# Performance work log

Hardware: AMD Instinct MI355X
Metric: run time of the kernel (lower is better)

Reference implementation:

```python
import jax, jax.numpy as jnp
import numpy as np

NUM_HEADS = 16

def setup_inputs() -> dict:
    key = jax.random.key(0)
    k1, k2, k3 = jax.random.split(key, 3)
    B, T, C = 4, 2048, 2048
    x = jax.random.normal(k1, (B, T, C), dtype=jnp.float32)
    Wqkv = jax.random.normal(k2, (C, 3 * C), dtype=jnp.float32) * (C ** -0.5)
    bqkv = jnp.zeros((3 * C,), dtype=jnp.float32)
    Wproj = jax.random.normal(k3, (C, C), dtype=jnp.float32) * (C ** -0.5)
    bproj = jnp.zeros((C,), dtype=jnp.float32)
    return {"x": x, "Wqkv": Wqkv, "bqkv": bqkv, "Wproj": Wproj, "bproj": bproj}

def reference(x, Wqkv, bqkv, Wproj, bproj):
    B, T, C = x.shape
    H = NUM_HEADS
    D = C // H  # head_dim
    qkv = x @ Wqkv + bqkv                      # [B,T,3C]
    q, k, v = jnp.split(qkv, 3, axis=-1)
    # [B,T,C] -> [B,H,T,D]
    q = q.reshape(B, T, H, D).transpose(0, 2, 1, 3)
    k = k.reshape(B, T, H, D).transpose(0, 2, 1, 3)
    v = v.reshape(B, T, H, D).transpose(0, 2, 1, 3)
    scale = D ** -0.5
    scores = jnp.einsum('bhqd,bhkd->bhqk', q, k) * scale  # [B,H,T,T]
    causal = jnp.tril(jnp.ones((T, T), dtype=bool))
    scores = jnp.where(causal, scores, jnp.finfo(scores.dtype).min)
    attn = jax.nn.softmax(scores, axis=-1)
    out = jnp.einsum('bhqk,bhkd->bhqd', attn, v)           # [B,H,T,D]
    out = out.transpose(0, 2, 1, 3).reshape(B, T, C)
    return out @ Wproj + bproj
```

## Files before the change

kernel.cpp:

```cpp
#include <hip/hip_runtime.h>
#include <hip/hip_bf16.h>
#include <stdint.h>

typedef __attribute__((ext_vector_type(8))) short short8;
typedef __attribute__((ext_vector_type(4))) float f32x4;
typedef __attribute__((ext_vector_type(16))) float f32x16;
typedef __attribute__((ext_vector_type(2))) unsigned int uint2v;

__device__ __forceinline__ unsigned short f2bf(float f) {
  union { float f; unsigned int u; } v; v.f = f;
  unsigned int r = v.u + 0x7FFFu + ((v.u >> 16) & 1u);
  return (unsigned short)(r >> 16);
}

__device__ __forceinline__ unsigned int cvtpk(float lo, float hi) {
  unsigned int r;
  asm("v_cvt_pk_bf16_f32 %0, %1, %2" : "=v"(r) : "v"(lo), "v"(hi));
  return r;
}

#define GLOAD16(gsrc, ldst)                                                                  \
  __builtin_amdgcn_global_load_lds((const __attribute__((address_space(1))) void*)(gsrc),    \
                                   (__attribute__((address_space(3))) void*)(ldst), 16, 0, 0)

#define BAR() __builtin_amdgcn_s_barrier()
#define LGKM0() do { asm volatile("s_waitcnt lgkmcnt(0)" ::: "memory"); \
                     __builtin_amdgcn_sched_barrier(0); } while (0)
#define VMCNT0() asm volatile("s_waitcnt vmcnt(0)" ::: "memory")
#define VMCNT8() asm volatile("s_waitcnt vmcnt(8)" ::: "memory")
#define PRIO(x) __builtin_amdgcn_s_setprio(x)

__global__ __launch_bounds__(256) void cast_bf16_kernel(const float* __restrict__ in,
                                                        unsigned short* __restrict__ out) {
  int i = blockIdx.x * 256 + threadIdx.x;
  float4 v = ((const float4*)in)[i];
  ushort4 o;
  o.x = f2bf(v.x); o.y = f2bf(v.y); o.z = f2bf(v.z); o.w = f2bf(v.w);
  ((ushort4*)out)[i] = o;
}

__global__ __launch_bounds__(256) void transpose_cast_kernel(const float* __restrict__ W,
                                                             unsigned short* __restrict__ Wt,
                                                             int K, int N) {
  __shared__ float tile[32][33];
  int n0 = blockIdx.x * 32, k0 = blockIdx.y * 32;
  int tx = threadIdx.x, ty = threadIdx.y;
#pragma unroll
  for (int j = 0; j < 32; j += 8)
    tile[ty + j][tx] = W[(size_t)(k0 + ty + j) * N + n0 + tx];
  __syncthreads();
#pragma unroll
  for (int j = 0; j < 32; j += 8)
    Wt[(size_t)(n0 + ty + j) * K + k0 + tx] = f2bf(tile[tx][ty + j]);
}

__device__ __forceinline__ void stage_half(const unsigned short* __restrict__ gp, int K,
                                           int kt, int half, char* lds_mat, int tid) {
#pragma unroll
  for (int it = 0; it < 2; ++it) {
    int li = half * 1024 + it * 512 + tid;
    int r = li >> 3, c = li & 7;
    int cs = c ^ (r & 7);
    GLOAD16(gp + (size_t)r * K + kt * 64 + cs * 8, lds_mat + li * 16);
  }
}

__device__ __forceinline__ void gemm256_mainloop(const unsigned short* __restrict__ Ap,
                                                 const unsigned short* __restrict__ Bp,
                                                 int K, int tid, char* smem,
                                                 f32x4 acc[8][4]) {
  char* sa = smem;
  char* sb = smem + 65536;
  const int KT = K >> 6;

  int wid = tid >> 6, lane = tid & 63;
  int wr = wid >> 2, wc = wid & 3;
  int lg = lane >> 4, l15 = lane & 15;
  int swz7 = l15 & 7;

  stage_half(Bp, K, 0, 0, sb, tid);
  stage_half(Bp, K, 0, 1, sb, tid);
  stage_half(Ap, K, 0, 0, sa, tid);
  stage_half(Ap, K, 0, 1, sa, tid);
  stage_half(Bp, K, 1, 0, sb + 32768, tid);
  stage_half(Bp, K, 1, 1, sb + 32768, tid);
  stage_half(Ap, K, 1, 0, sa + 32768, tid);
  stage_half(Ap, K, 1, 1, sa + 32768, tid);
  VMCNT8();
  BAR();

#define LDA(ab, m, kc) \
  (*(const short8*)((ab) + (size_t)((wr * 128 + (m) * 16 + l15) * 64 + ((((kc) * 4 + lg) ^ swz7) * 8))))
#define LDB(bb, n, kc) \
  (*(const short8*)((bb) + (size_t)((wc * 64 + (n) * 16 + l15) * 64 + ((((kc) * 4 + lg) ^ swz7) * 8))))

  for (int t = 0; t < KT; ++t) {
    int p = t & 1;
    const unsigned short* ab = (const unsigned short*)(sa + p * 32768);
    const unsigned short* bb = (const unsigned short*)(sb + p * 32768);
    int kt2 = (t + 2 < KT) ? t + 2 : KT - 1;

    short8 bq[4][2], aq[4][2], aq2[4][2];
#pragma unroll
    for (int n = 0; n < 4; ++n) { bq[n][0] = LDB(bb, n, 0); bq[n][1] = LDB(bb, n, 1); }
#pragma unroll
    for (int m = 0; m < 4; ++m) { aq[m][0] = LDA(ab, m, 0); aq[m][1] = LDA(ab, m, 1); }
    BAR();
    LGKM0();
    PRIO(1);
#pragma unroll
    for (int kc = 0; kc < 2; ++kc)
#pragma unroll
      for (int m = 0; m < 4; ++m)
#pragma unroll
        for (int n = 0; n < 2; ++n)
          acc[m][n] = __builtin_amdgcn_mfma_f32_16x16x32_bf16(aq[m][kc], bq[n][kc], acc[m][n], 0, 0, 0);
    PRIO(0);
    BAR();

    stage_half(Bp, K, kt2, 0, sb + p * 32768, tid);
#pragma unroll
    for (int m = 0; m < 4; ++m) { aq2[m][0] = LDA(ab, m + 4, 0); aq2[m][1] = LDA(ab, m + 4, 1); }
    PRIO(1);
#pragma unroll
    for (int kc = 0; kc < 2; ++kc)
#pragma unroll
      for (int m = 0; m < 4; ++m)
#pragma unroll
        for (int n = 2; n < 4; ++n)
          acc[m][n] = __builtin_amdgcn_mfma_f32_16x16x32_bf16(aq[m][kc], bq[n][kc], acc[m][n], 0, 0, 0);
    PRIO(0);

    stage_half(Bp, K, kt2, 1, sb + p * 32768, tid);
    LGKM0();
    PRIO(1);
#pragma unroll
    for (int kc = 0; kc < 2; ++kc)
#pragma unroll
      for (int m = 0; m < 4; ++m)
#pragma unroll
        for (int n = 2; n < 4; ++n)
          acc[m + 4][n] = __builtin_amdgcn_mfma_f32_16x16x32_bf16(aq2[m][kc], bq[n][kc], acc[m + 4][n], 0, 0, 0);
    PRIO(0);
    BAR();

    stage_half(Ap, K, kt2, 0, sa + p * 32768, tid);
    stage_half(Ap, K, kt2, 1, sa + p * 32768, tid);
    PRIO(1);
#pragma unroll
    for (int kc = 0; kc < 2; ++kc)
#pragma unroll
      for (int m = 0; m < 4; ++m)
#pragma unroll
        for (int n = 0; n < 2; ++n)
          acc[m + 4][n] = __builtin_amdgcn_mfma_f32_16x16x32_bf16(aq2[m][kc], bq[n][kc], acc[m + 4][n], 0, 0, 0);
    PRIO(0);
    VMCNT8();
    BAR();
  }
#undef LDA
#undef LDB
}

__global__ __launch_bounds__(512, 2) void gemm_qkv256_kernel(const unsigned short* __restrict__ A,
                                                             const unsigned short* __restrict__ Bt,
                                                             const float* __restrict__ bias,
                                                             unsigned short* __restrict__ qb,
                                                             unsigned short* __restrict__ kb,
                                                             unsigned short* __restrict__ vtb) {
  extern __shared__ char smem[];
  int wg = blockIdx.x;
  int xcd = wg & 7, idx = wg >> 3;
  int bn = xcd * 3 + idx % 3;
  int bm = idx / 3;
  int tid = threadIdx.x;

  f32x4 acc[8][4];
  f32x4 zero = {0.f, 0.f, 0.f, 0.f};
#pragma unroll
  for (int m = 0; m < 8; ++m)
#pragma unroll
    for (int n = 0; n < 4; ++n) acc[m][n] = zero;

  gemm256_mainloop(A + (size_t)bm * 256 * 2048, Bt + (size_t)bn * 256 * 2048, 2048, tid, smem, acc);

  const float QSCALE = (float)(0.08838834764831845 * 1.4426950408889634);
  int wid = tid >> 6, lane = tid & 63;
  int wr = wid >> 2, wc = wid & 3, lg = lane >> 4, l15 = lane & 15;
  int l31 = lane & 31, hi = lane >> 5;

  if (bn >= 16) {
    VMCNT0();
    BAR();
#pragma unroll
    for (int n = 0; n < 4; ++n) {
      int cl = wc * 64 + n * 16 + l15;
      float bv = bias[bn * 256 + cl];
#pragma unroll
      for (int m = 0; m < 8; ++m) {
        int rl = wr * 128 + m * 16 + lg * 4;
        unsigned int w0 = cvtpk(acc[m][n][0] + bv, acc[m][n][1] + bv);
        unsigned int w1 = cvtpk(acc[m][n][2] + bv, acc[m][n][3] + bv);
        uint2v pk = {w0, w1};
        *(uint2v*)(smem + cl * 512 + ((rl * 2) ^ ((cl & 7) << 4))) = pk;
      }
    }
    LGKM0();
    BAR();
    int t0_abs = bm * 256;
    int bq_ = t0_abs >> 11, t0 = t0_abs & 2047;
    int h0 = (bn * 256 - 4096) >> 7;
#pragma unroll
    for (int i = 0; i < 16; ++i) {
      int dloc = i * 16 + wid * 2 + hi;
      short8 vrow = *(const short8*)(smem + dloc * 512 + ((l31 * 16) ^ ((dloc & 7) << 4)));
      int bh_ = bq_ * 16 + h0 + (dloc >> 7);
      int d = dloc & 127;
      *(short8*)(vtb + ((size_t)bh_ * 128 + d) * 2048 + t0 + l31 * 8) = vrow;
    }
  } else {
#pragma unroll
    for (int n = 0; n < 4; ++n) {
      int col = bn * 256 + wc * 64 + n * 16 + l15;
      float bv = bias[col];
      int which = col >> 11;
      int h = (col & 2047) >> 7;
      int d = col & 127;
#pragma unroll
      for (int m = 0; m < 8; ++m) {
#pragma unroll
        for (int g = 0; g < 4; ++g) {
          int row = bm * 256 + wr * 128 + m * 16 + lg * 4 + g;
          int b = row >> 11, t = row & 2047;
          float r = acc[m][n][g] + bv;
          if (which == 0) r *= QSCALE;
          unsigned short val = f2bf(r);
          size_t bhi = (size_t)(b * 16 + h);
          if (which == 0) qb[(bhi * 2048 + t) * 128 + d] = val;
          else            kb[(bhi * 2048 + t) * 128 + d] = val;
        }
      }
    }
  }
}

__global__ __launch_bounds__(512, 2) void gemm_proj256_kernel(const unsigned short* __restrict__ A,
                                                              const unsigned short* __restrict__ Bt,
                                                              const float* __restrict__ bias,
                                                              float* __restrict__ out) {
  extern __shared__ char smem[];
  int wg = blockIdx.x;
  int bm = wg >> 3, bn = wg & 7;
  int tid = threadIdx.x;

  f32x4 acc[8][4];
  f32x4 zero = {0.f, 0.f, 0.f, 0.f};
#pragma unroll
  for (int m = 0; m < 8; ++m)
#pragma unroll
    for (int n = 0; n < 4; ++n) acc[m][n] = zero;

  gemm256_mainloop(A + (size_t)bm * 256 * 2048, Bt + (size_t)bn * 256 * 2048, 2048, tid, smem, acc);

  int wid = tid >> 6, lane = tid & 63;
  int wr = wid >> 2, wc = wid & 3, lg = lane >> 4, l15 = lane & 15;
#pragma unroll
  for (int n = 0; n < 4; ++n) {
    int col = bn * 256 + wc * 64 + n * 16 + l15;
    float bv = bias[col];
#pragma unroll
    for (int m = 0; m < 8; ++m) {
#pragma unroll
      for (int g = 0; g < 4; ++g) {
        int row = bm * 256 + wr * 128 + m * 16 + lg * 4 + g;
        out[(size_t)row * 2048 + col] = acc[m][n][g] + bv;
      }
    }
  }
}

__global__ __launch_bounds__(256) void attn_kernel(const unsigned short* __restrict__ qb,
                                                   const unsigned short* __restrict__ kb,
                                                   const unsigned short* __restrict__ vtb,
                                                   unsigned short* __restrict__ ob) {
  extern __shared__ char asmem[];
  int pairi = blockIdx.x;
  int bh = blockIdx.y;
  int b = bh >> 4, h = bh & 15;
  int tid = threadIdx.x, wid = tid >> 6, lane = tid & 63;
  int l31 = lane & 31, hi = lane >> 5;

  const unsigned short* Q  = qb  + (size_t)bh * 2048 * 128;
  const unsigned short* K  = kb  + (size_t)bh * 2048 * 128;
  const unsigned short* Vt = vtb + (size_t)bh * 128 * 2048;

#pragma unroll 1
  for (int pass = 0; pass < 2; ++pass) {
    int qt = pass == 0 ? (15 - pairi) : pairi;
    int NT = 2 * qt + 2;
    int qbase = qt * 128 + wid * 32;
    int qrow = qbase + l31;

    short8 qf[8];
#pragma unroll
    for (int kc = 0; kc < 8; ++kc)
      qf[kc] = *(const short8*)(Q + (size_t)qrow * 128 + kc * 16 + hi * 8);

    f32x16 o0 = {}, o1 = {}, o2 = {}, o3 = {};
    float m_run = -1e30f, l_run = 0.f;

    {
      char* kb_ = asmem;
#pragma unroll
      for (int it = 0; it < 4; ++it) {
        int li = it * 256 + tid;
        int r = li >> 4, c = li & 15;
        GLOAD16(K + (size_t)r * 128 + (c ^ (r & 7)) * 8, kb_ + li * 16);
      }
#pragma unroll
      for (int it = 0; it < 4; ++it) {
        int li = it * 256 + tid;
        int r = li >> 3, c = li & 7;
        GLOAD16(Vt + (size_t)r * 2048 + (c ^ (r & 7)) * 8, kb_ + 16384 + li * 16);
      }
    }
    VMCNT0();
    BAR();

#pragma unroll 1
    for (int kt = 0; kt < NT; ++kt) {
      char* cb = asmem + ((kt & 1) << 15);
      if (kt + 1 < NT) {
        char* nb = asmem + (((kt + 1) & 1) << 15);
        int kt1 = kt + 1;
#pragma unroll
        for (int it = 0; it < 4; ++it) {
          int li = it * 256 + tid;
          int r = li >> 4, c = li & 15;
          GLOAD16(K + (size_t)(kt1 * 64 + r) * 128 + (c ^ (r & 7)) * 8, nb + li * 16);
        }
#pragma unroll
        for (int it = 0; it < 4; ++it) {
          int li = it * 256 + tid;
          int r = li >> 3, c = li & 7;
          GLOAD16(Vt + (size_t)r * 2048 + kt1 * 64 + (c ^ (r & 7)) * 8, nb + 16384 + li * 16);
        }
      }

      bool active = (kt * 64 <= qbase + 31);
      if (active) {
        const char* k_l = cb;
        const char* v_l = cb + 16384;

        f32x16 s0v = {}, s1v = {};
        PRIO(1);
#pragma unroll
        for (int kc = 0; kc < 8; ++kc) {
          int cg = kc * 2 + hi;
          int sw = l31 & 7;
          short8 kf0 = *(const short8*)(k_l + l31 * 256 + ((cg ^ sw) * 16));
          s0v = __builtin_amdgcn_mfma_f32_32x32x16_bf16(kf0, qf[kc], s0v, 0, 0, 0);
          short8 kf1 = *(const short8*)(k_l + (32 + l31) * 256 + ((cg ^ sw) * 16));
          s1v = __builtin_amdgcn_mfma_f32_32x32x16_bf16(kf1, qf[kc], s1v, 0, 0, 0);
        }
        PRIO(0);

        if (kt * 64 + 63 > qbase) {
          int kvb = kt * 64 + 4 * hi;
#pragma unroll
          for (int r = 0; r < 16; ++r) {
            int kv = kvb + (r & 3) + 8 * (r >> 2);
            if (kv > qrow) s0v[r] = -1e30f;
            if (kv + 32 > qrow) s1v[r] = -1e30f;
          }
        }

        float tmax[16];
#pragma unroll
        for (int i = 0; i < 16; ++i) tmax[i] = fmaxf(s0v[i], s1v[i]);
#pragma unroll
        for (int st = 8; st >= 1; st >>= 1)
#pragma unroll
          for (int i = 0; i < st; ++i) tmax[i] = fmaxf(tmax[i], tmax[i + st]);
        float pmax = fmaxf(tmax[0], __shfl_xor(tmax[0], 32));

        if (!__all(pmax <= m_run + 8.0f)) {
          float mn = fmaxf(m_run, pmax);
          float alpha = exp2f(m_run - mn);
          m_run = mn; l_run *= alpha;
          o0 *= alpha; o1 *= alpha; o2 *= alpha; o3 *= alpha;
        }

#pragma unroll
        for (int i = 0; i < 16; ++i) {
          s0v[i] = exp2f(s0v[i] - m_run);
          s1v[i] = exp2f(s1v[i] - m_run);
        }
        float tsum[16];
#pragma unroll
        for (int i = 0; i < 16; ++i) tsum[i] = s0v[i] + s1v[i];
#pragma unroll
        for (int st = 8; st >= 1; st >>= 1)
#pragma unroll
          for (int i = 0; i < st; ++i) tsum[i] += tsum[i + st];
        float rsum = tsum[0] + __shfl_xor(tsum[0], 32);
        l_run += rsum;

#define BUILD_PA(sv, base, out)                                                \
        {                                                                      \
          unsigned int a_ = cvtpk(sv[base + 0], sv[base + 1]);                 \
          unsigned int c_ = cvtpk(sv[base + 2], sv[base + 3]);                 \
          unsigned int b_ = cvtpk(sv[base + 4], sv[base + 5]);                 \
          unsigned int d_ = cvtpk(sv[base + 6], sv[base + 7]);                 \
          uint2v r0_ = __builtin_amdgcn_permlane32_swap(a_, b_, false, false); \
          uint2v r1_ = __builtin_amdgcn_permlane32_swap(c_, d_, false, false); \
          union { unsigned int u[4]; short8 v; } uu_;                          \
          uu_.u[0] = r0_[0]; uu_.u[1] = r1_[0]; uu_.u[2] = r0_[1]; uu_.u[3] = r1_[1]; \
          out = uu_.v;                                                         \
        }
        short8 pa0, pa1, pa2, pa3;
        BUILD_PA(s0v, 0, pa0);
        BUILD_PA(s0v, 8, pa1);
        BUILD_PA(s1v, 0, pa2);
        BUILD_PA(s1v, 8, pa3);
#undef BUILD_PA

        PRIO(1);
#define PV_STEP(ovar, dt)                                                          \
        {                                                                          \
          int rv_ = dt * 32 + l31;                                                 \
          const char* vb_ = v_l + rv_ * 128;                                       \
          int sw_ = rv_ & 7;                                                       \
          short8 v0_ = *(const short8*)(vb_ + (((0 + hi) ^ sw_) * 16));            \
          ovar = __builtin_amdgcn_mfma_f32_32x32x16_bf16(v0_, pa0, ovar, 0, 0, 0); \
          short8 v1_ = *(const short8*)(vb_ + (((2 + hi) ^ sw_) * 16));            \
          ovar = __builtin_amdgcn_mfma_f32_32x32x16_bf16(v1_, pa1, ovar, 0, 0, 0); \
          short8 v2_ = *(const short8*)(vb_ + (((4 + hi) ^ sw_) * 16));            \
          ovar = __builtin_amdgcn_mfma_f32_32x32x16_bf16(v2_, pa2, ovar, 0, 0, 0); \
          short8 v3_ = *(const short8*)(vb_ + (((6 + hi) ^ sw_) * 16));            \
          ovar = __builtin_amdgcn_mfma_f32_32x32x16_bf16(v3_, pa3, ovar, 0, 0, 0); \
        }
        PV_STEP(o0, 0)
        PV_STEP(o1, 1)
        PV_STEP(o2, 2)
        PV_STEP(o3, 3)
#undef PV_STEP
        PRIO(0);
      }

      VMCNT0();
      BAR();
    }

    float inv = 1.0f / l_run;
    size_t orow = (size_t)(b * 2048 + qt * 128 + wid * 32 + l31);
    unsigned short* ob_p = ob + orow * 2048 + h * 128;
#define STORE_DT(ovar, dt)                                                         \
    {                                                                              \
      _Pragma("unroll")                                                            \
      for (int rq = 0; rq < 4; ++rq) {                                             \
        unsigned int w0 = cvtpk(ovar[rq * 4 + 0] * inv, ovar[rq * 4 + 1] * inv);   \
        unsigned int w1 = cvtpk(ovar[rq * 4 + 2] * inv, ovar[rq * 4 + 3] * inv);   \
        uint2v st = {w0, w1};                                                      \
        *(uint2v*)(ob_p + dt * 32 + rq * 8 + 4 * hi) = st;                         \
      }                                                                            \
    }
    STORE_DT(o0, 0)
    STORE_DT(o1, 1)
    STORE_DT(o2, 2)
    STORE_DT(o3, 3)
#undef STORE_DT
  }
}

extern "C" void kernel_launch(void* const* d_in, const int* in_sizes, int n_in,
                              void* d_out, int out_size, void* d_ws, size_t ws_size,
                              hipStream_t stream) {
  const float* x     = (const float*)d_in[0];
  const float* Wqkv  = (const float*)d_in[1];
  const float* bqkv  = (const float*)d_in[2];
  const float* Wproj = (const float*)d_in[3];
  const float* bproj = (const float*)d_in[4];
  float* out = (float*)d_out;

  char* ws = (char*)d_ws;
  unsigned short* x_bf   = (unsigned short*)ws;
  unsigned short* wqkvt  = (unsigned short*)(ws + 33554432);
  unsigned short* wprojt = (unsigned short*)(ws + 33554432 + 25165824);
  unsigned short* qb     = (unsigned short*)(ws + 67108864);
  unsigned short* kb     = (unsigned short*)(ws + 100663296);
  unsigned short* vtb    = (unsigned short*)(ws + 134217728);

  (void)hipFuncSetAttribute((const void*)gemm_qkv256_kernel,
                            hipFuncAttributeMaxDynamicSharedMemorySize, 131072);
  (void)hipFuncSetAttribute((const void*)gemm_proj256_kernel,
                            hipFuncAttributeMaxDynamicSharedMemorySize, 131072);
  (void)hipFuncSetAttribute((const void*)attn_kernel,
                            hipFuncAttributeMaxDynamicSharedMemorySize, 65536);

  cast_bf16_kernel<<<16384, 256, 0, stream>>>(x, x_bf);
  transpose_cast_kernel<<<dim3(192, 64), dim3(32, 8), 0, stream>>>(Wqkv, wqkvt, 2048, 6144);
  transpose_cast_kernel<<<dim3(64, 64), dim3(32, 8), 0, stream>>>(Wproj, wprojt, 2048, 2048);
  gemm_qkv256_kernel<<<768, 512, 131072, stream>>>(x_bf, wqkvt, bqkv, qb, kb, vtb);
  attn_kernel<<<dim3(8, 64), 256, 65536, stream>>>(qb, kb, vtb, x_bf );
  gemm_proj256_kernel<<<256, 512, 131072, stream>>>(x_bf, wprojt, bproj, out);
}
```

Measured before the change: 467.3 us.

## Restructure GEMM mainloop with cross-iteration register prefetch and staggered A/B staging

Reworks the 256-tile GEMM main loop so that the next tile's A and B0/1 fragments are read from LDS at the end of each iteration and carried across the loop. A is now staged one tile ahead instead of two, while B stays two ahead. Partial lgkmcnt waits and a vmcnt(4) wait replace full waits, so LDS reads and global-to-LDS copies overlap the MFMA quadrants more finely. The cost is more live registers and a tighter ordering dependence that could add stalls or race risk if the wait counts are wrong.

New measurement: 506.8 us. +8.5%, slower.

```diff
diff --git a/kernel.cpp b/kernel.cpp
--- a/kernel.cpp
+++ b/kernel.cpp
@@ -24,11 +24,14 @@
                                    (__attribute__((address_space(3))) void*)(ldst), 16, 0, 0)
 
 #define BAR() __builtin_amdgcn_s_barrier()
-#define LGKM0() do { asm volatile("s_waitcnt lgkmcnt(0)" ::: "memory"); \
-                     __builtin_amdgcn_sched_barrier(0); } while (0)
+#define LGKMC(n) do { asm volatile("s_waitcnt lgkmcnt(" #n ")" ::: "memory"); \
+                      __builtin_amdgcn_sched_barrier(0); } while (0)
+#define LGKM0() LGKMC(0)
 #define VMCNT0() asm volatile("s_waitcnt vmcnt(0)" ::: "memory")
-#define VMCNT8() asm volatile("s_waitcnt vmcnt(8)" ::: "memory")
+#define VMCNT4() do { asm volatile("s_waitcnt vmcnt(4)" ::: "memory"); \
+                      __builtin_amdgcn_sched_barrier(0); } while (0)
 #define PRIO(x) __builtin_amdgcn_s_setprio(x)
+#define MFMA16(d, a, b) d = __builtin_amdgcn_mfma_f32_16x16x32_bf16(a, b, d, 0, 0, 0)
 
 __global__ __launch_bounds__(256) void cast_bf16_kernel(const float* __restrict__ in,
                                                         unsigned short* __restrict__ out) {
@@ -78,35 +81,64 @@
   int lg = lane >> 4, l15 = lane & 15;
   int swz7 = l15 & 7;
 
+#define LDA(ab, m, kc) \
+  (*(const short8*)((const unsigned short*)(ab) + (size_t)((wr * 128 + (m) * 16 + l15) * 64 + ((((kc) * 4 + lg) ^ swz7) * 8))))
+#define LDB(bb, n, kc) \
+  (*(const short8*)((const unsigned short*)(bb) + (size_t)((wc * 64 + (n) * 16 + l15) * 64 + ((((kc) * 4 + lg) ^ swz7) * 8))))
+
   stage_half(Bp, K, 0, 0, sb, tid);
   stage_half(Bp, K, 0, 1, sb, tid);
   stage_half(Ap, K, 0, 0, sa, tid);
   stage_half(Ap, K, 0, 1, sa, tid);
   stage_half(Bp, K, 1, 0, sb + 32768, tid);
   stage_half(Bp, K, 1, 1, sb + 32768, tid);
-  stage_half(Ap, K, 1, 0, sa + 32768, tid);
-  stage_half(Ap, K, 1, 1, sa + 32768, tid);
-  VMCNT8();
+  VMCNT4();
   BAR();
 
-#define LDA(ab, m, kc) \
-  (*(const short8*)((ab) + (size_t)((wr * 128 + (m) * 16 + l15) * 64 + ((((kc) * 4 + lg) ^ swz7) * 8))))
-#define LDB(bb, n, kc) \
-  (*(const short8*)((bb) + (size_t)((wc * 64 + (n) * 16 + l15) * 64 + ((((kc) * 4 + lg) ^ swz7) * 8))))
+  short8 aq[4][2], aq2[4][2], bq01[2][2], bq23[2][2];
+#pragma unroll
+  for (int m = 0; m < 4; ++m) { aq[m][0] = LDA(sa, m, 0); aq[m][1] = LDA(sa, m, 1); }
+#pragma unroll
+  for (int n = 0; n < 2; ++n) { bq01[n][0] = LDB(sb, n, 0); bq01[n][1] = LDB(sb, n, 1); }
 
   for (int t = 0; t < KT; ++t) {
-    int p = t & 1;
-    const unsigned short* ab = (const unsigned short*)(sa + p * 32768);
-    const unsigned short* bb = (const unsigned short*)(sb + p * 32768);
+    int p = t & 1, pn = p ^ 1;
+    const char* ab = sa + p * 32768;
+    const char* bb = sb + p * 32768;
+    int kt1 = (t + 1 < KT) ? t + 1 : KT - 1;
     int kt2 = (t + 2 < KT) ? t + 2 : KT - 1;
 
-    short8 bq[4][2], aq[4][2], aq2[4][2];
-#pragma unroll
-    for (int n = 0; n < 4; ++n) { bq[n][0] = LDB(bb, n, 0); bq[n][1] = LDB(bb, n, 1); }
-#pragma unroll
-    for (int m = 0; m < 4; ++m) { aq[m][0] = LDA(ab, m, 0); aq[m][1] = LDA(ab, m, 1); }
+#pragma unroll
+    for (int n = 0; n < 2; ++n) { bq23[n][0] = LDB(bb, n + 2, 0); bq23[n][1] = LDB(bb, n + 2, 1); }
+    stage_half(Ap, K, kt1, 1, sa + pn * 32768, tid);
+    LGKMC(4);
+    PRIO(1);
+#pragma unroll
+    for (int kc = 0; kc < 2; ++kc)
+#pragma unroll
+      for (int m = 0; m < 4; ++m)
+#pragma unroll
+        for (int n = 0; n < 2; ++n)
+          MFMA16(acc[m][n], aq[m][kc], bq01[n][kc]);
+    PRIO(0);
+
+#pragma unroll
+    for (int m = 0; m < 4; ++m) { aq2[m][0] = LDA(ab, m + 4, 0); aq2[m][1] = LDA(ab, m + 4, 1); }
+    stage_half(Ap, K, kt1, 0, sa + pn * 32768, tid);
+    LGKMC(8);
+    PRIO(1);
+#pragma unroll
+    for (int kc = 0; kc < 2; ++kc)
+#pragma unroll
+      for (int m = 0; m < 4; ++m)
+#pragma unroll
+        for (int n = 0; n < 2; ++n)
+          MFMA16(acc[m][n + 2], aq[m][kc], bq23[n][kc]);
+    PRIO(0);
+
     BAR();
-    LGKM0();
+    stage_half(Bp, K, kt2, 0, sb + p * 32768, tid);
+    LGKMC(0);
     PRIO(1);
 #pragma unroll
     for (int kc = 0; kc < 2; ++kc)
@@ -114,48 +146,29 @@
       for (int m = 0; m < 4; ++m)
 #pragma unroll
         for (int n = 0; n < 2; ++n)
-          acc[m][n] = __builtin_amdgcn_mfma_f32_16x16x32_bf16(aq[m][kc], bq[n][kc], acc[m][n], 0, 0, 0);
+          MFMA16(acc[m + 4][n + 2], aq2[m][kc], bq23[n][kc]);
     PRIO(0);
+
+    stage_half(Bp, K, kt2, 1, sb + p * 32768, tid);
+    VMCNT4();
     BAR();
-
-    stage_half(Bp, K, kt2, 0, sb + p * 32768, tid);
-#pragma unroll
-    for (int m = 0; m < 4; ++m) { aq2[m][0] = LDA(ab, m + 4, 0); aq2[m][1] = LDA(ab, m + 4, 1); }
     PRIO(1);
 #pragma unroll
     for (int kc = 0; kc < 2; ++kc)
 #pragma unroll
       for (int m = 0; m < 4; ++m)
 #pragma unroll
-        for (int n = 2; n < 4; ++n)
-          acc[m][n] = __builtin_amdgcn_mfma_f32_16x16x32_bf16(aq[m][kc], bq[n][kc], acc[m][n], 0, 0, 0);
+        for (int n = 0; n < 2; ++n)
+          MFMA16(acc[m + 4][n], aq2[m][kc], bq01[n][kc]);
     PRIO(0);
-
-    stage_half(Bp, K, kt2, 1, sb + p * 32768, tid);
-    LGKM0();
-    PRIO(1);
-#pragma unroll
-    for (int kc = 0; kc < 2; ++kc)
-#pragma unroll
-      for (int m = 0; m < 4; ++m)
-#pragma unroll
-        for (int n = 2; n < 4; ++n)
-          acc[m + 4][n] = __builtin_amdgcn_mfma_f32_16x16x32_bf16(aq2[m][kc], bq[n][kc], acc[m + 4][n], 0, 0, 0);
-    PRIO(0);
-    BAR();
-
-    stage_half(Ap, K, kt2, 0, sa + p * 32768, tid);
-    stage_half(Ap, K, kt2, 1, sa + p * 32768, tid);
-    PRIO(1);
-#pragma unroll
-    for (int kc = 0; kc < 2; ++kc)
-#pragma unroll
-      for (int m = 0; m < 4; ++m)
-#pragma unroll
-        for (int n = 0; n < 2; ++n)
-          acc[m + 4][n] = __builtin_amdgcn_mfma_f32_16x16x32_bf16(aq2[m][kc], bq[n][kc], acc[m + 4][n], 0, 0, 0);
-    PRIO(0);
-    VMCNT8();
+    {
+      const char* abn = sa + pn * 32768;
+      const char* bbn = sb + pn * 32768;
+#pragma unroll
+      for (int m = 0; m < 4; ++m) { aq[m][0] = LDA(abn, m, 0); aq[m][1] = LDA(abn, m, 1); }
+#pragma unroll
+      for (int n = 0; n < 2; ++n) { bq01[n][0] = LDB(bbn, n, 0); bq01[n][1] = LDB(bbn, n, 1); }
+    }
     BAR();
   }
 #undef LDA
```
